# Kernel optimization log

Measured on AMD Instinct MI355X. Metric: run time of the kernel, lower is better.

## Reference

```python
import jax, jax.numpy as jnp
import numpy as np

TOPK = 13
NUM_CLASSES = 80
ALPHA = 1.0
BETA = 6.0
EPS = 1e-9
BS, NA, NMAX = 16, 8400, 64
IMG = 640


def _anchor_grid():
    pts = []
    for s in (8, 16, 32):
        n = IMG // s
        yv, xv = jnp.meshgrid(jnp.arange(n, dtype=jnp.float32), jnp.arange(n, dtype=jnp.float32), indexing='ij')
        pts.append(jnp.stack([(xv + 0.5) * s, (yv + 0.5) * s], -1).reshape(-1, 2))
    return jnp.concatenate(pts, 0)  # (8400, 2)


def setup_inputs() -> dict:
    key = jax.random.key(0)
    ks = jax.random.split(key, 6)
    pd_scores = jax.nn.sigmoid(jax.random.normal(ks[0], (BS, NA, NUM_CLASSES), jnp.float32))
    # predicted circles: centers in image, radii in [4, 68]
    pxy = jax.random.uniform(ks[1], (BS, NA, 2), jnp.float32) * IMG
    pr = jax.random.uniform(ks[1], (BS, NA, 1), jnp.float32) * 64.0 + 4.0
    pd_circles = jnp.concatenate([pxy, pr], -1)
    anc_points = _anchor_grid()
    gt_labels = jax.random.randint(ks[2], (BS, NMAX, 1), 0, NUM_CLASSES, jnp.int32)
    gxy = jax.random.uniform(ks[3], (BS, NMAX, 2), jnp.float32) * IMG
    gr = jax.random.uniform(ks[3], (BS, NMAX, 1), jnp.float32) * 64.0 + 8.0
    gt_bboxes = jnp.concatenate([gxy, gr], -1)  # circles (x, y, r)
    n_valid = jax.random.randint(ks[4], (BS, 1), 8, NMAX + 1)
    mask_gt = (jnp.arange(NMAX)[None, :] < n_valid).astype(jnp.float32)[..., None]
    return {"pd_scores": pd_scores, "pd_circles": pd_circles, "anc_points": anc_points,
            "gt_labels": gt_labels, "gt_bboxes": gt_bboxes, "mask_gt": mask_gt}


def circle_iou(c1, c2, eps):
    # c1, c2: broadcastable (..., 3) = (x, y, r); IoU of two discs via lens area.
    d = jnp.sqrt(jnp.sum((c1[..., :2] - c2[..., :2]) ** 2, -1) + eps)
    r1, r2 = c1[..., 2], c2[..., 2]
    a1, a2 = jnp.pi * r1 ** 2, jnp.pi * r2 ** 2
    cos1 = jnp.clip((d ** 2 + r1 ** 2 - r2 ** 2) / (2.0 * d * r1 + eps), -1.0, 1.0)
    cos2 = jnp.clip((d ** 2 + r2 ** 2 - r1 ** 2) / (2.0 * d * r2 + eps), -1.0, 1.0)
    tri = jnp.clip((r1 + r2 - d) * (d + r1 - r2) * (d - r1 + r2) * (d + r1 + r2), 0.0)
    lens = r1 ** 2 * jnp.arccos(cos1) + r2 ** 2 * jnp.arccos(cos2) - 0.5 * jnp.sqrt(tri)
    inter = jnp.where(d >= r1 + r2, 0.0,
                      jnp.where(d <= jnp.abs(r1 - r2), jnp.pi * jnp.minimum(r1, r2) ** 2, lens))
    return inter / (a1 + a2 - inter + eps)


def reference(pd_scores, pd_circles, anc_points, gt_labels, gt_bboxes, mask_gt):
    bs, na, nc = pd_scores.shape
    n_max = gt_bboxes.shape[1]
    # ---- candidates inside GT circles: (b, n_max, na) ----
    dist = jnp.linalg.norm(gt_bboxes[:, :, None, :2] - anc_points[None, None, :, :], axis=-1)
    mask_in_gts = (dist <= gt_bboxes[:, :, None, 2]).astype(jnp.float32)
    mask_valid = mask_in_gts * mask_gt  # mask_gt (b, n_max, 1) broadcasts
    # ---- alignment metric ----
    labels = jnp.clip(gt_labels[..., 0], 0, nc - 1)  # (b, n_max)
    b_idx = jnp.arange(bs)[:, None, None]
    a_idx = jnp.arange(na)[None, None, :]
    bbox_scores = pd_scores[b_idx, a_idx, labels[:, :, None]] * mask_valid  # (b, n_max, na)
    overlaps = circle_iou(gt_bboxes[:, :, None, :], pd_circles[:, None, :, :], EPS) * mask_valid
    align_metric = bbox_scores ** ALPHA * overlaps ** BETA
    # ---- topk candidate selection with duplicate suppression ----
    _, topk_idxs = jax.lax.top_k(align_metric, TOPK)  # (b, n_max, TOPK)
    topk_idxs = jnp.where(mask_gt > 0, topk_idxs, 0)
    count = jnp.zeros((bs, n_max, na), jnp.float32).at[
        jnp.arange(bs)[:, None, None], jnp.arange(n_max)[None, :, None], topk_idxs].add(1.0)
    mask_topk = jnp.where(count > 1, 0.0, count)
    mask_pos = mask_topk * mask_in_gts * mask_gt  # (b, n_max, na)
    # ---- resolve anchors claimed by multiple GTs via max overlap ----
    fg_count = mask_pos.sum(1)  # (b, na)
    is_max = jax.nn.one_hot(overlaps.argmax(1), n_max, axis=1, dtype=jnp.float32)  # (b, n_max, na)
    mask_pos = jnp.where(fg_count[:, None, :] > 1, is_max, mask_pos)
    fg_mask = mask_pos.sum(1)  # (b, na)
    target_gt_idx = mask_pos.argmax(1)  # (b, na)
    # ---- gather targets ----
    target_labels = jnp.clip(jnp.take_along_axis(gt_labels[..., 0], target_gt_idx, axis=1), 0, None)
    target_circles = jnp.take_along_axis(gt_bboxes, target_gt_idx[..., None], axis=1)  # (b, na, 3)
    target_scores = jax.nn.one_hot(target_labels, nc, dtype=pd_scores.dtype)
    target_scores = target_scores * (fg_mask[..., None] > 0)
    # ---- normalize scores by aligned metric ----
    align_metric = align_metric * mask_pos
    pos_align = jnp.max(align_metric, -1, keepdims=True)  # (b, n_max, 1)
    pos_overlaps = jnp.max(overlaps * mask_pos, -1, keepdims=True)
    norm = jnp.max(align_metric * pos_overlaps / (pos_align + EPS), 1)[..., None]  # (b, na, 1)
    target_scores = target_scores * norm
    return target_labels, target_circles, target_scores, fg_mask, target_gt_idx
```

## Files before the change

### kernel.cpp

```cpp
#include <hip/hip_runtime.h>
#include <cmath>

#define NA 8400
#define NC 80
#define BS 16
#define NMAX 64
#define TOPKK 13
#define CAP 768
#define NN_REG 12
#define CEPS 1e-9f
#define PIF 3.14159265358979323846f

#define OFF_LABELS  0
#define OFF_CIRCLES 134400
#define OFF_SCORES  537600
#define OFF_FG      11289600
#define OFF_TGI     11424000

#define WS_OVKEY   1075200
#define WS_POSAL   2150400
#define WS_POSOV   2154496
#define WS_TGI     2158592
#define WS_ALIGN   2696192
#define ZERO_WS_F4 134912

__device__ __forceinline__ float circle_iou_dev(float gx, float gy, float r1,
                                                float px, float py, float r2) {
    float dx = gx - px, dy = gy - py;
    float d = sqrtf(dx * dx + dy * dy + CEPS);
    float a1 = PIF * r1 * r1, a2 = PIF * r2 * r2;
    float d2 = d * d;
    float c1 = (d2 + r1 * r1 - r2 * r2) / (2.0f * d * r1 + CEPS);
    float c2 = (d2 + r2 * r2 - r1 * r1) / (2.0f * d * r2 + CEPS);
    c1 = fminf(fmaxf(c1, -1.0f), 1.0f);
    c2 = fminf(fmaxf(c2, -1.0f), 1.0f);
    float tri = fmaxf((r1 + r2 - d) * (d + r1 - r2) * (d - r1 + r2) * (d + r1 + r2), 0.0f);
    float lens = r1 * r1 * acosf(c1) + r2 * r2 * acosf(c2) - 0.5f * sqrtf(tri);
    float inter;
    if (d >= r1 + r2)             inter = 0.0f;
    else if (d <= fabsf(r1 - r2)) { float rm = fminf(r1, r2); inter = PIF * rm * rm; }
    else                          inter = lens;
    return inter / (a1 + a2 - inter + CEPS);
}

__global__ __launch_bounds__(256) void k0_zero(float4* __restrict__ wsz)
{
    int i = blockIdx.x * 256 + threadIdx.x;
    if (i < ZERO_WS_F4) wsz[i] = make_float4(0.f, 0.f, 0.f, 0.f);
}

__global__ __launch_bounds__(256) void k1_topk(
    const float* __restrict__ pd_scores, const float* __restrict__ pd_circles,
    const int* __restrict__ gt_labels, const float* __restrict__ gt_bboxes,
    const float* __restrict__ mask_gt, unsigned long long* __restrict__ colbits,
    unsigned long long* __restrict__ ovkey)
{
    __shared__ int   s_cidx[CAP];
    __shared__ float s_cval[CAP];
    __shared__ float s_low[64];
    __shared__ int   s_ncand;

    const int row = blockIdx.x;
    const int b = row >> 6, j = row & 63;
    const int t = threadIdx.x;
    const int lane = t & 63, wv = t >> 6;

    if (mask_gt[row] <= 0.0f) return;

    const float gx = gt_bboxes[row * 3 + 0];
    const float gy = gt_bboxes[row * 3 + 1];
    const float gr = gt_bboxes[row * 3 + 2];
    int lab = gt_labels[row];
    lab = min(max(lab, 0), NC - 1);

    if (t == 0) s_ncand = 0;
    if (t < 64) s_low[t] = 0.0f;
    __syncthreads();

    unsigned long long m_ingt0 = 0ull;
    if (wv == 0) {
        float ax = ((float)lane + 0.5f) * 8.0f, ay = 4.0f;
        float dx = gx - ax, dy = gy - ay;
        m_ingt0 = __ballot(sqrtf(dx * dx + dy * dy) <= gr);
    }

    const int strides_[3] = {8, 16, 32};
    const int ns_[3]      = {80, 40, 20};
    const int bases_[3]   = {0, 6400, 8000};
#pragma unroll
    for (int l = 0; l < 3; ++l) {
        const float sl = (float)strides_[l];
        const int n_l = ns_[l], base_l = bases_[l];
        const float inv = 1.0f / sl;
        int y0 = (int)ceilf((gy - gr) * inv - 0.5f) - 1;
        int y1 = (int)floorf((gy + gr) * inv - 0.5f) + 1;
        int x0 = (int)ceilf((gx - gr) * inv - 0.5f) - 1;
        int x1 = (int)floorf((gx + gr) * inv - 0.5f) + 1;
        y0 = max(y0, 0); x0 = max(x0, 0);
        y1 = min(y1, n_l - 1); x1 = min(x1, n_l - 1);
        const int W = x1 - x0 + 1, H = y1 - y0 + 1;
        if (W > 0 && H > 0) {
            const int cells = W * H;
            const int kk = (cells + 255) >> 8;
            for (int k = 0; k < kk; ++k) {
                const int c = k * 256 + t;
                bool found = false; int aidx = 0;
                if (c < cells) {
                    const int q = c / W;
                    const int iy = y0 + q, ix = x0 + (c - q * W);
                    float ax = ((float)ix + 0.5f) * sl;
                    float ay = ((float)iy + 0.5f) * sl;
                    float dx = gx - ax, dy = gy - ay;
                    found = (sqrtf(dx * dx + dy * dy) <= gr);
                    aidx = base_l + iy * n_l + ix;
                }
                unsigned long long m = __ballot(found);
                if (m) {
                    const int cnt = __popcll(m);
                    const int ldr = __ffsll(m) - 1;
                    int base = 0;
                    if (lane == ldr) base = atomicAdd(&s_ncand, cnt);
                    base = __shfl(base, ldr);
                    if (found) {
                        int p = base + __popcll(m & ((1ull << lane) - 1ull));
                        if (p < CAP) s_cidx[p] = aidx;
                    }
                }
            }
        }
    }
    __syncthreads();
    const int n = min(s_ncand, CAP);

    for (int c = t; c < n; c += 256) {
        int a = s_cidx[c];
        size_t pi = (size_t)(b * NA + a);
        float px = pd_circles[pi * 3 + 0];
        float py = pd_circles[pi * 3 + 1];
        float pr = pd_circles[pi * 3 + 2];
        float iou = circle_iou_dev(gx, gy, gr, px, py, pr);
        float sc  = pd_scores[pi * NC + lab];
        float o2 = iou * iou;
        float v = sc * (o2 * o2 * o2);
        s_cval[c] = v;
        if (a < 64) s_low[a] = v;
        unsigned long long key =
            ((unsigned long long)__float_as_uint(iou) << 32) |
            (unsigned long long)(63 - j);
        atomicMax(&ovkey[(size_t)b * NA + a], key);
    }
    __syncthreads();

    if (wv != 0) return;

    float rv[NN_REG]; int ri[NN_REG];
#pragma unroll
    for (int s = 0; s < NN_REG; ++s) {
        int c = s * 64 + lane;
        bool ok = (c < n);
        rv[s] = ok ? s_cval[c] : -1.0f;
        ri[s] = ok ? s_cidx[c] : (1 << 30);
    }

    int selv[TOPKK];
#pragma unroll
    for (int s = 0; s < TOPKK; ++s) selv[s] = 0;
    int nsel = 0;

    for (int it = 0; it < TOPKK; ++it) {
        float bv = -1.0f; int bi = 1 << 30;
#pragma unroll
        for (int s = 0; s < NN_REG; ++s)
            if (rv[s] > bv || (rv[s] == bv && ri[s] < bi)) { bv = rv[s]; bi = ri[s]; }
        for (int off = 32; off > 0; off >>= 1) {
            float ov = __shfl_xor(bv, off);
            int   oi = __shfl_xor(bi, off);
            if (ov > bv || (ov == bv && oi < bi)) { bv = ov; bi = oi; }
        }
        if (bv <= 0.0f) break;
#pragma unroll
        for (int s = 0; s < TOPKK; ++s) if (s == nsel) selv[s] = bi;
        nsel++;
#pragma unroll
        for (int s = 0; s < NN_REG; ++s) if (ri[s] == bi) rv[s] = -1.0f;
    }

    {
        float lowv = s_low[lane];
        unsigned long long mpos = __ballot(lowv > 0.0f);
        unsigned long long zeros = ~mpos;
        int r = TOPKK - nsel;
        while (r > 0 && zeros) {
            int idx = __ffsll(zeros) - 1;
            zeros &= zeros - 1ull;
            r--;
            if ((m_ingt0 >> idx) & 1ull) {
#pragma unroll
                for (int s = 0; s < TOPKK; ++s) if (s == nsel) selv[s] = idx;
                nsel++;
            }
        }
    }

    if (lane == 0) {
#pragma unroll
        for (int s = 0; s < TOPKK; ++s)
            if (s < nsel)
                atomicOr(&colbits[(size_t)b * NA + selv[s]], 1ull << j);
    }
}

__global__ __launch_bounds__(256) void k2_resolve(
    const float* __restrict__ pd_scores, const float* __restrict__ pd_circles,
    const float* __restrict__ anc, const int* __restrict__ gt_labels,
    const float* __restrict__ gt_bboxes, const float* __restrict__ mask_gt,
    const unsigned long long* __restrict__ colbits,
    const unsigned long long* __restrict__ ovkey,
    float* __restrict__ out, int* __restrict__ tgiE, float* __restrict__ alignv,
    unsigned int* __restrict__ posal, unsigned int* __restrict__ posov)
{
    const int idx = blockIdx.x * 256 + threadIdx.x;
    const int b = idx / NA;
    const int a = idx - b * NA;

    const unsigned long long col = colbits[idx];
    const int cnt = __popcll(col);

    int tgi = 0, fg = 0;
    if (cnt == 1) { fg = 1; tgi = __ffsll((unsigned long long)col) - 1; }
    else if (cnt > 1) {
        fg = 1;
        const unsigned long long key = ovkey[idx];
        const unsigned int ib = (unsigned int)(key >> 32);
        tgi = (ib != 0u) ? (63 - (int)(key & 63ull)) : 0;
    }

    const int gl = gt_labels[b * NMAX + tgi];
    const float gx = gt_bboxes[(b * NMAX + tgi) * 3 + 0];
    const float gy = gt_bboxes[(b * NMAX + tgi) * 3 + 1];
    const float gr = gt_bboxes[(b * NMAX + tgi) * 3 + 2];

    out[OFF_LABELS + idx] = (float)max(gl, 0);
    out[OFF_CIRCLES + (size_t)idx * 3 + 0] = gx;
    out[OFF_CIRCLES + (size_t)idx * 3 + 1] = gy;
    out[OFF_CIRCLES + (size_t)idx * 3 + 2] = gr;
    out[OFF_FG + idx]  = (float)fg;
    out[OFF_TGI + idx] = (float)tgi;
    tgiE[idx] = fg ? tgi : -1;

    float alg = 0.0f;
    if (fg) {
        float ovv = 0.0f;
        float mgv = mask_gt[b * NMAX + tgi];
        float ax = anc[2 * a], ay = anc[2 * a + 1];
        float dx = gx - ax, dy = gy - ay;
        if (mgv > 0.0f && sqrtf(dx * dx + dy * dy) <= gr) {
            float px = pd_circles[(size_t)idx * 3 + 0];
            float py = pd_circles[(size_t)idx * 3 + 1];
            float pr = pd_circles[(size_t)idx * 3 + 2];
            float iou = circle_iou_dev(gx, gy, gr, px, py, pr);
            int lab = min(max(gl, 0), NC - 1);
            float sc = pd_scores[((size_t)b * NA + a) * NC + lab];
            ovv = iou;
            float o2 = iou * iou;
            alg = sc * (o2 * o2 * o2);
        }
        atomicMax(&posal[b * NMAX + tgi], __float_as_uint(alg));
        atomicMax(&posov[b * NMAX + tgi], __float_as_uint(ovv));
    }
    alignv[idx] = alg;
}

__global__ __launch_bounds__(256) void k4_dense(
    const int* __restrict__ tgiE, const float* __restrict__ alignv,
    const unsigned int* __restrict__ posal, const unsigned int* __restrict__ posov,
    const int* __restrict__ gt_labels, float4* __restrict__ scores4)
{
    const int f = blockIdx.x * 256 + threadIdx.x;
    const int a_idx = f / 20;
    const int p = f - a_idx * 20;

    float4 v = make_float4(0.f, 0.f, 0.f, 0.f);
    const int tg = tgiE[a_idx];
    if (tg >= 0) {
        const int b = a_idx / NA;
        const float pa = __uint_as_float(posal[b * NMAX + tg]);
        const float po = __uint_as_float(posov[b * NMAX + tg]);
        const float norm = alignv[a_idx] * po / (pa + CEPS);
        const int lab = max(gt_labels[b * NMAX + tg], 0);
        if ((lab >> 2) == p) ((float*)&v)[lab & 3] = norm;
    }
    scores4[f] = v;
}

extern "C" void kernel_launch(void* const* d_in, const int* in_sizes, int n_in,
                              void* d_out, int out_size, void* d_ws, size_t ws_size,
                              hipStream_t stream) {
    const float* pd_scores  = (const float*)d_in[0];
    const float* pd_circles = (const float*)d_in[1];
    const float* anc        = (const float*)d_in[2];
    const int*   gt_labels  = (const int*)d_in[3];
    const float* gt_bboxes  = (const float*)d_in[4];
    const float* mask_gt    = (const float*)d_in[5];
    float* out = (float*)d_out;

    char* ws = (char*)d_ws;
    unsigned long long* colbits = (unsigned long long*)ws;
    unsigned long long* ovkey   = (unsigned long long*)(ws + WS_OVKEY);
    unsigned int* posal = (unsigned int*)(ws + WS_POSAL);
    unsigned int* posov = (unsigned int*)(ws + WS_POSOV);
    int*   tgiE   = (int*)(ws + WS_TGI);
    float* alignv = (float*)(ws + WS_ALIGN);

    k0_zero<<<(ZERO_WS_F4 + 255) / 256, 256, 0, stream>>>((float4*)ws);
    k1_topk<<<BS * NMAX, 256, 0, stream>>>(pd_scores, pd_circles, gt_labels,
                                           gt_bboxes, mask_gt, colbits, ovkey);
    k2_resolve<<<(BS * NA) / 256, 256, 0, stream>>>(pd_scores, pd_circles, anc,
                                                    gt_labels, gt_bboxes, mask_gt,
                                                    colbits, ovkey, out, tgiE,
                                                    alignv, posal, posov);
    k4_dense<<<(BS * NA * NC / 4) / 256, 256, 0, stream>>>(tgiE, alignv, posal,
                                                           posov, gt_labels,
                                                           (float4*)(out + OFF_SCORES));
}
```

Measured before the change: 152.8 us.

## Split top-k selection across four wavefronts with a shared-memory merge

Top-k selection now runs in two stages. Each of the four wavefronts first picks its own 13 best candidates from a 192-entry chunk using 3 registers per lane. Wave 0 then merges the 52 partial winners with one value per lane. Candidate compaction switches from ballot-aggregated atomics to per-thread shared atomics, and the final colbits atomicOr calls are spread over lanes instead of all issuing from lane 0. The aim is to shorten the serial selection loop on a single wavefront, at the cost of an extra block barrier and more contention on the shared candidate counter.

```diff
diff --git a/kernel.cpp b/kernel.cpp
--- a/kernel.cpp
+++ b/kernel.cpp
@@ -7,7 +7,8 @@
 #define NMAX 64
 #define TOPKK 13
 #define CAP 768
-#define NN_REG 12
+#define CHUNK 192
+#define NW_REG 3
 #define CEPS 1e-9f
 #define PIF 3.14159265358979323846f
 
@@ -59,6 +60,8 @@
     __shared__ float s_cval[CAP];
     __shared__ float s_low[64];
     __shared__ int   s_ncand;
+    __shared__ float s_mv[4 * TOPKK];
+    __shared__ int   s_mi[4 * TOPKK];
 
     const int row = blockIdx.x;
     const int b = row >> 6, j = row & 63;
@@ -101,30 +104,15 @@
         const int W = x1 - x0 + 1, H = y1 - y0 + 1;
         if (W > 0 && H > 0) {
             const int cells = W * H;
-            const int kk = (cells + 255) >> 8;
-            for (int k = 0; k < kk; ++k) {
-                const int c = k * 256 + t;
-                bool found = false; int aidx = 0;
-                if (c < cells) {
-                    const int q = c / W;
-                    const int iy = y0 + q, ix = x0 + (c - q * W);
-                    float ax = ((float)ix + 0.5f) * sl;
-                    float ay = ((float)iy + 0.5f) * sl;
-                    float dx = gx - ax, dy = gy - ay;
-                    found = (sqrtf(dx * dx + dy * dy) <= gr);
-                    aidx = base_l + iy * n_l + ix;
-                }
-                unsigned long long m = __ballot(found);
-                if (m) {
-                    const int cnt = __popcll(m);
-                    const int ldr = __ffsll(m) - 1;
-                    int base = 0;
-                    if (lane == ldr) base = atomicAdd(&s_ncand, cnt);
-                    base = __shfl(base, ldr);
-                    if (found) {
-                        int p = base + __popcll(m & ((1ull << lane) - 1ull));
-                        if (p < CAP) s_cidx[p] = aidx;
-                    }
+            for (int c = t; c < cells; c += 256) {
+                const int q = c / W;
+                const int iy = y0 + q, ix = x0 + (c - q * W);
+                float ax = ((float)ix + 0.5f) * sl;
+                float ay = ((float)iy + 0.5f) * sl;
+                float dx = gx - ax, dy = gy - ay;
+                if (sqrtf(dx * dx + dy * dy) <= gr) {
+                    int p = atomicAdd(&s_ncand, 1);
+                    if (p < CAP) s_cidx[p] = base_l + iy * n_l + ix;
                 }
             }
         }
@@ -151,16 +139,39 @@
     }
     __syncthreads();
 
+    float myv = -1.0f; int myi = 1 << 30;
+    {
+        float rv[NW_REG]; int ri[NW_REG];
+#pragma unroll
+        for (int r = 0; r < NW_REG; ++r) {
+            int c = wv * CHUNK + r * 64 + lane;
+            bool ok = (c < n);
+            rv[r] = ok ? s_cval[c] : -1.0f;
+            ri[r] = ok ? s_cidx[c] : (1 << 30);
+        }
+        for (int it = 0; it < TOPKK; ++it) {
+            float bv = rv[0]; int bi = ri[0];
+#pragma unroll
+            for (int r = 1; r < NW_REG; ++r)
+                if (rv[r] > bv || (rv[r] == bv && ri[r] < bi)) { bv = rv[r]; bi = ri[r]; }
+            for (int off = 32; off > 0; off >>= 1) {
+                float ov = __shfl_xor(bv, off);
+                int   oi = __shfl_xor(bi, off);
+                if (ov > bv || (ov == bv && oi < bi)) { bv = ov; bi = oi; }
+            }
+            if (bv <= 0.0f) break;
+            if (lane == it) { myv = bv; myi = bi; }
+#pragma unroll
+            for (int r = 0; r < NW_REG; ++r) if (ri[r] == bi) rv[r] = -1.0f;
+        }
+    }
+    if (lane < TOPKK) { s_mv[wv * TOPKK + lane] = myv; s_mi[wv * TOPKK + lane] = myi; }
+    __syncthreads();
+
     if (wv != 0) return;
 
-    float rv[NN_REG]; int ri[NN_REG];
-#pragma unroll
-    for (int s = 0; s < NN_REG; ++s) {
-        int c = s * 64 + lane;
-        bool ok = (c < n);
-        rv[s] = ok ? s_cval[c] : -1.0f;
-        ri[s] = ok ? s_cidx[c] : (1 << 30);
-    }
+    float ev = -1.0f; int ei = 1 << 30;
+    if (lane < 4 * TOPKK) { ev = s_mv[lane]; ei = s_mi[lane]; }
 
     int selv[TOPKK];
 #pragma unroll
@@ -168,10 +179,7 @@
     int nsel = 0;
 
     for (int it = 0; it < TOPKK; ++it) {
-        float bv = -1.0f; int bi = 1 << 30;
-#pragma unroll
-        for (int s = 0; s < NN_REG; ++s)
-            if (rv[s] > bv || (rv[s] == bv && ri[s] < bi)) { bv = rv[s]; bi = ri[s]; }
+        float bv = ev; int bi = ei;
         for (int off = 32; off > 0; off >>= 1) {
             float ov = __shfl_xor(bv, off);
             int   oi = __shfl_xor(bi, off);
@@ -181,8 +189,7 @@
 #pragma unroll
         for (int s = 0; s < TOPKK; ++s) if (s == nsel) selv[s] = bi;
         nsel++;
-#pragma unroll
-        for (int s = 0; s < NN_REG; ++s) if (ri[s] == bi) rv[s] = -1.0f;
+        if (ei == bi) ev = -1.0f;
     }
 
     {
@@ -202,12 +209,10 @@
         }
     }
 
-    if (lane == 0) {
-#pragma unroll
-        for (int s = 0; s < TOPKK; ++s)
-            if (s < nsel)
-                atomicOr(&colbits[(size_t)b * NA + selv[s]], 1ull << j);
-    }
+#pragma unroll
+    for (int s = 0; s < TOPKK; ++s)
+        if (lane == s && s < nsel)
+            atomicOr(&colbits[(size_t)b * NA + selv[s]], 1ull << j);
 }
 
 __global__ __launch_bounds__(256) void k2_resolve(
```

New measurement: 152.8 us. Within noise of the previous version (+0.1%).
